# Kernel optimization log

Measured on AMD Instinct MI355X. Metric: run time of the kernel, lower is better.

Reference implementation:

```python
import jax, jax.numpy as jnp
import numpy as np

IN_C, OUT_C, K, N_FILTERS, STRIDE, PAD = 256, 512, 3, 64, 1, 1


def setup_inputs() -> dict:
    key = jax.random.key(0)
    kx, kw, kb, krw, krb = jax.random.split(key, 5)
    fan_in = IN_C * K * K
    bound = 1.0 / np.sqrt(fan_in)
    x = jax.random.normal(kx, (32, IN_C, 56, 56), dtype=jnp.float32)
    weight = jax.random.uniform(kw, (OUT_C, IN_C, K, K), minval=-bound, maxval=bound, dtype=jnp.float32)
    bias = jax.random.uniform(kb, (OUT_C,), minval=-bound, maxval=bound, dtype=jnp.float32)
    rbound = 1.0 / np.sqrt(IN_C)
    router_w = jax.random.uniform(krw, (OUT_C, IN_C), minval=-rbound, maxval=rbound, dtype=jnp.float32)
    router_b = jax.random.uniform(krb, (OUT_C,), minval=-rbound, maxval=rbound, dtype=jnp.float32)
    return {"x": x, "weight": weight, "bias": bias, "router_w": router_w, "router_b": router_b}


def reference(x, weight, bias, router_w, router_b):
    B = x.shape[0]
    # router: global avg pool -> linear -> top-k channel mask
    pooled = jnp.mean(x, axis=(2, 3))                      # [B, IN_C]
    router_out = pooled @ router_w.T + router_b            # [B, OUT_C]
    _, top_idx = jax.lax.top_k(router_out, N_FILTERS)      # [B, k]
    mask = jnp.zeros((B, OUT_C), dtype=x.dtype).at[jnp.arange(B)[:, None], top_idx].set(1.0)
    # dense conv2d
    conv = jax.lax.conv_general_dilated(
        x, weight, window_strides=(STRIDE, STRIDE), padding=[(PAD, PAD), (PAD, PAD)],
        dimension_numbers=("NCHW", "OIHW", "NCHW"))
    conv = conv + bias[None, :, None, None]
    return conv * mask[:, :, None, None]
```

## Files before the change

### kernel.cpp

```cpp
#include <hip/hip_runtime.h>

#define IN_C   256
#define OUT_C  512
#define WIDTH  56
#define HW     3136
#define KTOT   2304
#define NF     64
#define NU     448
#define NB     32
#define NGRP   8
#define TN     128
#define NTILE  25
#define XROWS  242
#define LDX    40

typedef __bf16 bf16x8 __attribute__((ext_vector_type(8)));
typedef float  f32x4  __attribute__((ext_vector_type(4)));

__global__ __launch_bounds__(256) void pool_kernel(const float* __restrict__ x,
                                                   float* __restrict__ pooled) {
    int bc = blockIdx.x;
    const float* src = x + (size_t)bc * HW;
    float s = 0.f;
    for (int i = threadIdx.x; i < HW; i += 256) s += src[i];
    #pragma unroll
    for (int off = 32; off > 0; off >>= 1) s += __shfl_down(s, off, 64);
    __shared__ float wsum[4];
    int lane = threadIdx.x & 63, wv = threadIdx.x >> 6;
    if (lane == 0) wsum[wv] = s;
    __syncthreads();
    if (threadIdx.x == 0)
        pooled[bc] = (wsum[0] + wsum[1] + wsum[2] + wsum[3]) * (1.0f / HW);
}

__global__ __launch_bounds__(512) void router_kernel(const float* __restrict__ pooled,
                                                     const float* __restrict__ rw,
                                                     const float* __restrict__ rb,
                                                     int* __restrict__ sel,
                                                     int* __restrict__ unsel) {
    int b = blockIdx.x;
    __shared__ float p[IN_C];
    __shared__ float v[OUT_C];
    __shared__ int   scount, ucount;
    int t = threadIdx.x;
    if (t < IN_C) p[t] = pooled[b * IN_C + t];
    if (t == 0) { scount = 0; ucount = 0; }
    __syncthreads();
    float acc = rb[t];
    const float* wrow = rw + (size_t)t * IN_C;
    for (int i = 0; i < IN_C; ++i) acc += p[i] * wrow[i];
    v[t] = acc;
    __syncthreads();
    int cnt = 0;
    for (int j = 0; j < OUT_C; ++j) {
        float o = v[j];
        cnt += (o > acc) || (o == acc && j < t);
    }
    if (cnt < NF) {
        int pos = atomicAdd(&scount, 1);
        sel[b * NF + pos] = t;
    } else {
        int pos = atomicAdd(&ucount, 1);
        unsel[b * NU + pos] = t;
    }
}

__global__ __launch_bounds__(256) void compact_w(const float* __restrict__ w,
                                                 const int* __restrict__ sel,
                                                 __bf16* __restrict__ Acomp) {
    int id = blockIdx.x;
    int b = id / 72, rem = id - b * 72;
    int g = rem / 9, tap = rem - g * 9;
    int t = threadIdx.x;
    int oc = t >> 2, q = t & 3;
    int s = sel[b * NF + oc];
    const float* wsrc = w + (size_t)s * KTOT + tap;
    bf16x8 o;
    #pragma unroll
    for (int j = 0; j < 8; ++j)
        o[j] = (__bf16)wsrc[(g * 32 + q * 8 + j) * 9];
    *(bf16x8*)&Acomp[((size_t)id * 64 + oc) * 32 + q * 8] = o;
}

__global__ __launch_bounds__(256, 4) void conv_kernel(const float* __restrict__ x,
                                                      const __bf16* __restrict__ Acomp,
                                                      const float* __restrict__ bias,
                                                      const int* __restrict__ sel,
                                                      const int* __restrict__ unsel,
                                                      float* __restrict__ out) {
    int id   = blockIdx.x;
    int xcd  = id & 7, slot = id >> 3;
    int bq   = slot / NTILE;
    int tile = slot - bq * NTILE;
    int b    = xcd * 4 + bq;
    int ptile = tile * TN;

    int t    = threadIdx.x;
    int lane = t & 63, wv = t >> 6;
    int fm   = lane & 15, fq = lane >> 4;
    int n_base = wv * 32;

    __shared__ __bf16 xlds[2][XROWS * LDX];

    const float*  x_b    = x + (size_t)b * IN_C * HW;
    const __bf16* a_base = Acomp + (size_t)b * (NGRP * 9 * 64 * 32);

    int pp[2], poh[2], pow_[2];
    #pragma unroll
    for (int s = 0; s < 2; ++s) {
        int p = ptile + n_base + s * 16 + fm;
        pp[s] = p;
        int pc = p < HW ? p : HW - 1;
        poh[s]  = pc / WIDTH;
        pow_[s] = pc - poh[s] * WIDTH;
    }

    int  sp   = t;
    bool sact = sp < XROWS;
    int  gp   = ptile - 57 + sp;
    gp = gp < 0 ? 0 : (gp > HW - 1 ? HW - 1 : gp);
    const float* sx = x_b + gp;

    if (sact) {
        #pragma unroll
        for (int oct = 0; oct < 4; ++oct) {
            float v[8];
            #pragma unroll
            for (int j = 0; j < 8; ++j) v[j] = sx[(size_t)(oct * 8 + j) * HW];
            bf16x8 o;
            #pragma unroll
            for (int j = 0; j < 8; ++j) o[j] = (__bf16)v[j];
            *(bf16x8*)&xlds[0][sp * LDX + oct * 8] = o;
        }
    }
    __syncthreads();

    f32x4 acc[4][2] = {};
    float pre[32];

    for (int g = 0; g < NGRP; ++g) {
        int cur = g & 1;
        if (g < NGRP - 1 && sact) {
            #pragma unroll
            for (int i = 0; i < 32; ++i)
                pre[i] = sx[(size_t)((g + 1) * 32 + i) * HW];
        }
        const __bf16* gp_a = a_base + (size_t)g * 9 * 64 * 32;
        #pragma unroll
        for (int t9 = 0; t9 < 9; ++t9) {
            const int r = t9 / 3, c = t9 - 3 * (t9 / 3);
            const int shift = (r - 1) * WIDTH + (c - 1);
            const __bf16* ap = gp_a + (size_t)t9 * 64 * 32;
            bf16x8 af[4];
            #pragma unroll
            for (int mi = 0; mi < 4; ++mi)
                af[mi] = *(const bf16x8*)(ap + (size_t)(mi * 16 + fm) * 32 + fq * 8);
            #pragma unroll
            for (int s = 0; s < 2; ++s) {
                int ohr = poh[s] + r - 1, owc = pow_[s] + c - 1;
                bool ok = ((unsigned)ohr < 56u) && ((unsigned)owc < 56u);
                int n = n_base + s * 16 + fm;
                bf16x8 bfr = *(const bf16x8*)&xlds[cur][(n + 57 + shift) * LDX + fq * 8];
                bf16x8 z = {};
                bfr = ok ? bfr : z;
                #pragma unroll
                for (int mi = 0; mi < 4; ++mi)
                    acc[mi][s] = __builtin_amdgcn_mfma_f32_16x16x32_bf16(af[mi], bfr, acc[mi][s], 0, 0, 0);
            }
        }
        if (g < NGRP - 1) {
            if (sact) {
                #pragma unroll
                for (int oct = 0; oct < 4; ++oct) {
                    bf16x8 o;
                    #pragma unroll
                    for (int j = 0; j < 8; ++j) o[j] = (__bf16)pre[oct * 8 + j];
                    *(bf16x8*)&xlds[cur ^ 1][sp * LDX + oct * 8] = o;
                }
            }
            __syncthreads();
        }
    }

    const int* selb = sel + b * NF;
    size_t outb = (size_t)b * OUT_C * HW;
    #pragma unroll
    for (int mi = 0; mi < 4; ++mi) {
        #pragma unroll
        for (int reg = 0; reg < 4; ++reg) {
            int m  = mi * 16 + fq * 4 + reg;
            int oc = selb[m];
            float bs = bias[oc];
            float* orow = out + outb + (size_t)oc * HW;
            #pragma unroll
            for (int s = 0; s < 2; ++s)
                if (pp[s] < HW) orow[pp[s]] = acc[mi][s][reg] + bs;
        }
    }

    {
        const int* unselb = unsel + b * NU;
        int j = t & 31;
        bool jok = (ptile + j * 4) < HW;
        float4 z = {0.f, 0.f, 0.f, 0.f};
        for (int u = t >> 5; u < NU; u += 8) {
            int oc = unselb[u];
            if (jok)
                *(float4*)(out + outb + (size_t)oc * HW + ptile + j * 4) = z;
        }
    }
}

extern "C" void kernel_launch(void* const* d_in, const int* in_sizes, int n_in,
                              void* d_out, int out_size, void* d_ws, size_t ws_size,
                              hipStream_t stream) {
    (void)in_sizes; (void)n_in; (void)ws_size; (void)out_size;
    const float* x        = (const float*)d_in[0];
    const float* weight   = (const float*)d_in[1];
    const float* bias     = (const float*)d_in[2];
    const float* router_w = (const float*)d_in[3];
    const float* router_b = (const float*)d_in[4];
    float* out = (float*)d_out;

    char* ws = (char*)d_ws;
    float*  pooled = (float*)ws;
    int*    sel    = (int*)(ws + 32768);
    int*    unsel  = (int*)(ws + 40960);
    __bf16* Acomp  = (__bf16*)(ws + 131072);

    pool_kernel<<<NB * IN_C, 256, 0, stream>>>(x, pooled);
    router_kernel<<<NB, OUT_C, 0, stream>>>(pooled, router_w, router_b, sel, unsel);
    compact_w<<<NB * NGRP * 9, 256, 0, stream>>>(weight, sel, Acomp);

    conv_kernel<<<NTILE * NB, 256, 0, stream>>>(x, Acomp, bias, sel, unsel, out);
}
```

Before: 406.3 us.

## Restructure conv into single-wave 64-pixel tiles with nontemporal stores

The conv kernel now runs one 64-lane wave per block over 64-pixel tiles (49 tiles per image) instead of four waves over 128-pixel tiles. It drops the double-buffered LDS prefetch and the __syncthreads, so each wave loads its own x slab per channel group and then runs the MFMAs. Zero-fill of unselected channels moves to the start of the kernel, and both zero and result writes use nontemporal stores; the pool kernel also reads float4. The aim is more blocks and occupancy with no block barriers, at the cost of losing load/compute overlap within a wave and re-reading more halo rows of x.

```diff
diff --git a/kernel.cpp b/kernel.cpp
--- a/kernel.cpp
+++ b/kernel.cpp
@@ -9,9 +9,9 @@
 #define NU     448
 #define NB     32
 #define NGRP   8
-#define TN     128
-#define NTILE  25
-#define XROWS  242
+#define TN     64
+#define NTILE  49
+#define XROWS  178
 #define LDX    40
 
 typedef __bf16 bf16x8 __attribute__((ext_vector_type(8)));
@@ -20,9 +20,12 @@
 __global__ __launch_bounds__(256) void pool_kernel(const float* __restrict__ x,
                                                    float* __restrict__ pooled) {
     int bc = blockIdx.x;
-    const float* src = x + (size_t)bc * HW;
+    const float4* src = (const float4*)(x + (size_t)bc * HW);
     float s = 0.f;
-    for (int i = threadIdx.x; i < HW; i += 256) s += src[i];
+    for (int i = threadIdx.x; i < HW / 4; i += 256) {
+        float4 v = src[i];
+        s += v.x + v.y + v.z + v.w;
+    }
     #pragma unroll
     for (int off = 32; off > 0; off >>= 1) s += __shfl_down(s, off, 64);
     __shared__ float wsum[4];
@@ -82,12 +85,12 @@
     *(bf16x8*)&Acomp[((size_t)id * 64 + oc) * 32 + q * 8] = o;
 }
 
-__global__ __launch_bounds__(256, 4) void conv_kernel(const float* __restrict__ x,
-                                                      const __bf16* __restrict__ Acomp,
-                                                      const float* __restrict__ bias,
-                                                      const int* __restrict__ sel,
-                                                      const int* __restrict__ unsel,
-                                                      float* __restrict__ out) {
+__global__ __launch_bounds__(64) void conv_kernel(const float* __restrict__ x,
+                                                  const __bf16* __restrict__ Acomp,
+                                                  const float* __restrict__ bias,
+                                                  const int* __restrict__ sel,
+                                                  const int* __restrict__ unsel,
+                                                  float* __restrict__ out) {
     int id   = blockIdx.x;
     int xcd  = id & 7, slot = id >> 3;
     int bq   = slot / NTILE;
@@ -95,55 +98,63 @@
     int b    = xcd * 4 + bq;
     int ptile = tile * TN;
 
-    int t    = threadIdx.x;
-    int lane = t & 63, wv = t >> 6;
+    int lane = threadIdx.x;
     int fm   = lane & 15, fq = lane >> 4;
-    int n_base = wv * 32;
-
-    __shared__ __bf16 xlds[2][XROWS * LDX];
+
+    __shared__ __bf16 xlds[XROWS * LDX];
+
+    size_t outb = (size_t)b * OUT_C * HW;
+
+    {
+        const int* unselb = unsel + b * NU;
+        f32x4 z = {0.f, 0.f, 0.f, 0.f};
+        for (int u = fq; u < NU; u += 4) {
+            int oc = unselb[u];
+            __builtin_nontemporal_store(z, (f32x4*)(out + outb + (size_t)oc * HW + ptile) + fm);
+        }
+    }
 
     const float*  x_b    = x + (size_t)b * IN_C * HW;
     const __bf16* a_base = Acomp + (size_t)b * (NGRP * 9 * 64 * 32);
 
-    int pp[2], poh[2], pow_[2];
-    #pragma unroll
-    for (int s = 0; s < 2; ++s) {
-        int p = ptile + n_base + s * 16 + fm;
-        pp[s] = p;
-        int pc = p < HW ? p : HW - 1;
-        poh[s]  = pc / WIDTH;
-        pow_[s] = pc - poh[s] * WIDTH;
-    }
-
-    int  sp   = t;
-    bool sact = sp < XROWS;
-    int  gp   = ptile - 57 + sp;
-    gp = gp < 0 ? 0 : (gp > HW - 1 ? HW - 1 : gp);
-    const float* sx = x_b + gp;
-
-    if (sact) {
+    int pp[4], poh[4], pow_[4];
+    #pragma unroll
+    for (int s = 0; s < 4; ++s) {
+        int p = ptile + s * 16 + fm;
+        pp[s]   = p;
+        poh[s]  = p / WIDTH;
+        pow_[s] = p - poh[s] * WIDTH;
+    }
+
+    int gp0[3]; bool act[3];
+    #pragma unroll
+    for (int it = 0; it < 3; ++it) {
+        int sp = it * 64 + lane;
+        act[it] = sp < XROWS;
+        int gp = ptile - 57 + sp;
+        gp = gp < 0 ? 0 : (gp > HW - 1 ? HW - 1 : gp);
+        gp0[it] = gp;
+    }
+
+    f32x4 acc[4][4] = {};
+
+    #pragma unroll 1
+    for (int g = 0; g < NGRP; ++g) {
         #pragma unroll
-        for (int oct = 0; oct < 4; ++oct) {
-            float v[8];
-            #pragma unroll
-            for (int j = 0; j < 8; ++j) v[j] = sx[(size_t)(oct * 8 + j) * HW];
-            bf16x8 o;
-            #pragma unroll
-            for (int j = 0; j < 8; ++j) o[j] = (__bf16)v[j];
-            *(bf16x8*)&xlds[0][sp * LDX + oct * 8] = o;
-        }
-    }
-    __syncthreads();
-
-    f32x4 acc[4][2] = {};
-    float pre[32];
-
-    for (int g = 0; g < NGRP; ++g) {
-        int cur = g & 1;
-        if (g < NGRP - 1 && sact) {
-            #pragma unroll
-            for (int i = 0; i < 32; ++i)
-                pre[i] = sx[(size_t)((g + 1) * 32 + i) * HW];
+        for (int it = 0; it < 3; ++it) {
+            if (!act[it]) continue;
+            int sp = it * 64 + lane;
+            const float* sx = x_b + (size_t)(g * 32) * HW + gp0[it];
+            #pragma unroll
+            for (int oct = 0; oct < 4; ++oct) {
+                float v[8];
+                #pragma unroll
+                for (int j = 0; j < 8; ++j) v[j] = sx[(size_t)(oct * 8 + j) * HW];
+                bf16x8 o;
+                #pragma unroll
+                for (int j = 0; j < 8; ++j) o[j] = (__bf16)v[j];
+                *(bf16x8*)&xlds[sp * LDX + oct * 8] = o;
+            }
         }
         const __bf16* gp_a = a_base + (size_t)g * 9 * 64 * 32;
         #pragma unroll
@@ -156,57 +167,30 @@
             for (int mi = 0; mi < 4; ++mi)
                 af[mi] = *(const bf16x8*)(ap + (size_t)(mi * 16 + fm) * 32 + fq * 8);
             #pragma unroll
-            for (int s = 0; s < 2; ++s) {
+            for (int s = 0; s < 4; ++s) {
                 int ohr = poh[s] + r - 1, owc = pow_[s] + c - 1;
                 bool ok = ((unsigned)ohr < 56u) && ((unsigned)owc < 56u);
-                int n = n_base + s * 16 + fm;
-                bf16x8 bfr = *(const bf16x8*)&xlds[cur][(n + 57 + shift) * LDX + fq * 8];
-                bf16x8 z = {};
-                bfr = ok ? bfr : z;
+                bf16x8 bfr = *(const bf16x8*)&xlds[(s * 16 + fm + 57 + shift) * LDX + fq * 8];
+                bf16x8 zz = {};
+                bfr = ok ? bfr : zz;
                 #pragma unroll
                 for (int mi = 0; mi < 4; ++mi)
                     acc[mi][s] = __builtin_amdgcn_mfma_f32_16x16x32_bf16(af[mi], bfr, acc[mi][s], 0, 0, 0);
             }
         }
-        if (g < NGRP - 1) {
-            if (sact) {
-                #pragma unroll
-                for (int oct = 0; oct < 4; ++oct) {
-                    bf16x8 o;
-                    #pragma unroll
-                    for (int j = 0; j < 8; ++j) o[j] = (__bf16)pre[oct * 8 + j];
-                    *(bf16x8*)&xlds[cur ^ 1][sp * LDX + oct * 8] = o;
-                }
-            }
-            __syncthreads();
-        }
     }
 
     const int* selb = sel + b * NF;
-    size_t outb = (size_t)b * OUT_C * HW;
     #pragma unroll
     for (int mi = 0; mi < 4; ++mi) {
         #pragma unroll
         for (int reg = 0; reg < 4; ++reg) {
-            int m  = mi * 16 + fq * 4 + reg;
-            int oc = selb[m];
+            int oc = selb[mi * 16 + fq * 4 + reg];
             float bs = bias[oc];
             float* orow = out + outb + (size_t)oc * HW;
             #pragma unroll
-            for (int s = 0; s < 2; ++s)
-                if (pp[s] < HW) orow[pp[s]] = acc[mi][s][reg] + bs;
-        }
-    }
-
-    {
-        const int* unselb = unsel + b * NU;
-        int j = t & 31;
-        bool jok = (ptile + j * 4) < HW;
-        float4 z = {0.f, 0.f, 0.f, 0.f};
-        for (int u = t >> 5; u < NU; u += 8) {
-            int oc = unselb[u];
-            if (jok)
-                *(float4*)(out + outb + (size_t)oc * HW + ptile + j * 4) = z;
+            for (int s = 0; s < 4; ++s)
+                __builtin_nontemporal_store(acc[mi][s][reg] + bs, &orow[pp[s]]);
         }
     }
 }
@@ -232,5 +216,5 @@
     router_kernel<<<NB, OUT_C, 0, stream>>>(pooled, router_w, router_b, sel, unsel);
     compact_w<<<NB * NGRP * 9, 256, 0, stream>>>(weight, sel, Acomp);
 
-    conv_kernel<<<NTILE * NB, 256, 0, stream>>>(x, Acomp, bias, sel, unsel, out);
-}
+    conv_kernel<<<NTILE * NB, 64, 0, stream>>>(x, Acomp, bias, sel, unsel, out);
+}
```

Result: faster. 375.8 us (-7.5%).
